# Kernel optimization log

Hardware: AMD Instinct MI355X
Metric: run time of the kernel (lower is better)

## Reference

```python
import jax, jax.numpy as jnp
import numpy as np

DIM = 320
DIM_HEAD = 10
HEADS = DIM // DIM_HEAD
WH, WW = 8, 8  # window_size
EPS = 1e-12    # F.normalize eps


def setup_inputs() -> dict:
    key = jax.random.key(0)
    ks = jax.random.split(key, 9)
    B, H, W, C = 8, 128, 128, DIM
    s = 0.02
    return {
        "x": jax.random.normal(ks[0], (B, H, W, C), jnp.float32),
        "qkv_w": jax.random.normal(ks[1], (C, 3 * C), jnp.float32) * s,
        "qkv_b": jax.random.normal(ks[2], (3 * C,), jnp.float32) * s,
        "proj_w": jax.random.normal(ks[3], (C, C), jnp.float32) * s,
        "proj_b": jax.random.normal(ks[4], (C,), jnp.float32) * s,
        "gamma": jnp.full((C,), 1e-5, jnp.float32),
        "w1": jax.random.normal(ks[5], (C, 4 * C), jnp.float32) * s,  # bias=False
        "w2": jax.random.normal(ks[6], (4 * C, C), jnp.float32) * s,
        "b2": jax.random.normal(ks[7], (C,), jnp.float32) * s,
    }


def _l2norm(v):
    # F.normalize(x, dim=-1): x / max(||x||_2, eps)
    n = jnp.sqrt(jnp.sum(v * v, axis=-1, keepdims=True))
    return v / jnp.maximum(n, EPS)


def _block(x, qkv_w, qkv_b, proj_w, proj_b, gamma, w1, w2, b2):
    x = _l2norm(x)
    B, H, W, C = x.shape
    # window partition: (B,H,W,C) -> (nW, WH, WW, C)
    xw = x.reshape(B, H // WH, WH, W // WW, WW, C)
    xw = xw.transpose(0, 1, 3, 2, 4, 5).reshape(-1, WH, WW, C)
    nW = xw.shape[0]
    N = WH * WW
    # attention (matches torch view: channels grouped as (heads, 3*dim_head))
    qkv = xw.reshape(nW, N, C) @ qkv_w + qkv_b           # (nW, N, 3C)
    qkv = qkv.reshape(nW, N, HEADS, 3 * DIM_HEAD).transpose(0, 2, 1, 3)
    q, k, v = jnp.split(qkv, 3, axis=-1)                 # each (nW, h, N, dh)
    scores = jnp.einsum("whnd,whmd->whnm", q, k) * (DIM_HEAD ** -0.5)
    attn = jax.nn.softmax(scores, axis=-1)
    o = jnp.einsum("whnm,whmd->whnd", attn, v)
    o = o.transpose(0, 2, 1, 3).reshape(nW, N, C) @ proj_w + proj_b
    xw = xw + o.reshape(nW, WH, WW, C)
    # window reverse
    x = xw.reshape(B, H // WH, W // WW, WH, WW, C)
    x = x.transpose(0, 1, 3, 2, 4, 5).reshape(B, H, W, C)
    x = _l2norm(x)
    h = jax.nn.relu(x @ w1)                              # (B,H,W,4C)
    h = jax.nn.relu(h @ w2 + b2)
    return x + h * gamma                                 # layerscale


def reference(x, qkv_w, qkv_b, proj_w, proj_b, gamma, w1, w2, b2):
    return _block(x, qkv_w, qkv_b, proj_w, proj_b, gamma, w1, w2, b2)
```

## Files before the change

kernel.cpp:

```cpp
#include <hip/hip_runtime.h>
#include <cstdint>

typedef __bf16 bf16;
typedef __attribute__((ext_vector_type(8))) __bf16 bf16x8;
typedef __attribute__((ext_vector_type(4))) float f32x4;
typedef __attribute__((ext_vector_type(4))) uint32_t u32x4;
typedef __attribute__((ext_vector_type(2))) uint32_t u32x2;

#define MTOT (8*128*128)
#define MCH  16384

#define GLOAD16(g, l) __builtin_amdgcn_global_load_lds( \
    (const __attribute__((address_space(1))) unsigned int*)(g), \
    (__attribute__((address_space(3))) unsigned int*)(l), 16, 0, 0)

__global__ __launch_bounds__(256)
void transpose_cast_kernel(const float* __restrict__ in, bf16* __restrict__ out,
                           int R, int C) {
    __shared__ float tile[32][33];
    const int tx = threadIdx.x & 31, ty = threadIdx.x >> 5;
    const int c0 = blockIdx.x * 32, r0 = blockIdx.y * 32;
#pragma unroll
    for (int r = ty; r < 32; r += 8) tile[r][tx] = in[(size_t)(r0 + r) * C + c0 + tx];
    __syncthreads();
#pragma unroll
    for (int r = ty; r < 32; r += 8) out[(size_t)(c0 + r) * R + r0 + tx] = (bf16)tile[tx][r];
}

__global__ __launch_bounds__(256)
void l2norm_kernel(const float* __restrict__ X, bf16* __restrict__ O) {
    const int tid = threadIdx.x, wv = tid >> 6, lane = tid & 63;
    const size_t row = (size_t)blockIdx.x * 4 + wv;
    const float* xr = X + row * 320;
    bf16* orow = O + row * 320;
    float v[5];
    float ss = 0.f;
#pragma unroll
    for (int r = 0; r < 5; ++r) {
        v[r] = xr[r * 64 + lane];
        ss += v[r] * v[r];
    }
#pragma unroll
    for (int off = 32; off; off >>= 1) ss += __shfl_xor(ss, off);
    const float sc = 1.f / fmaxf(sqrtf(ss), 1e-12f);
#pragma unroll
    for (int r = 0; r < 5; ++r) orow[r * 64 + lane] = (bf16)(v[r] * sc);
}

template <int WM, int WN, int EPI, typename OutT>
__global__ __launch_bounds__(WM * WN * 64)
void gemm_kernel(const bf16* __restrict__ A, const bf16* __restrict__ WT,
                 const float* __restrict__ bias, const bf16* __restrict__ res,
                 const float* __restrict__ gamma, OutT* __restrict__ out,
                 int K, int N) {
    constexpr int T  = WM * WN * 64;
    constexpr int BM = WM * 64, BN = WN * 64;
    constexpr int GA = (BM * 4) / T;
    constexpr int GB = (BN * 4) / T;
    constexpr int RG = T / 4;
    __shared__ bf16 As[BM * 32];
    __shared__ bf16 Bs[BN * 32];
    const int tid = threadIdx.x;
    const int wv = tid >> 6, lane = tid & 63;
    const int wm = wv / WN, wn = wv % WN;
    const int n0 = blockIdx.x * BN, m0 = blockIdx.y * BM;
    const int r0 = lane & 15, qd = lane >> 4;

    f32x4 acc[4][4];
#pragma unroll
    for (int i = 0; i < 4; ++i)
#pragma unroll
        for (int j = 0; j < 4; ++j)
#pragma unroll
            for (int r = 0; r < 4; ++r) acc[i][j][r] = 0.f;

    const int sr = tid >> 2, sc = (tid & 3) << 3;
    const bf16* Ag = A  + (size_t)(m0 + sr) * K + sc;
    const bf16* Bg = WT + (size_t)(n0 + sr) * K + sc;
    bf16* Asw = As + tid * 8;
    bf16* Bsw = Bs + tid * 8;
    const bf16* ap = As + (wm * 64 + r0) * 32 + qd * 8;
    const bf16* bp = Bs + (wn * 64 + r0) * 32 + qd * 8;

    for (int kk = 0; kk < K; kk += 32) {
        __syncthreads();
#pragma unroll
        for (int g = 0; g < GA; ++g)
            GLOAD16(Ag + (size_t)(g * RG) * K + kk, Asw + g * (T * 8));
#pragma unroll
        for (int g = 0; g < GB; ++g)
            GLOAD16(Bg + (size_t)(g * RG) * K + kk, Bsw + g * (T * 8));
        __syncthreads();
        bf16x8 a[4], b[4];
#pragma unroll
        for (int i = 0; i < 4; ++i) a[i] = *(const bf16x8*)(ap + i * (16 * 32));
#pragma unroll
        for (int j = 0; j < 4; ++j) b[j] = *(const bf16x8*)(bp + j * (16 * 32));
#pragma unroll
        for (int j = 0; j < 4; ++j)
#pragma unroll
            for (int i = 0; i < 4; ++i)
                acc[i][j] = __builtin_amdgcn_mfma_f32_16x16x32_bf16(a[i], b[j], acc[i][j], 0, 0, 0);
    }

#pragma unroll
    for (int i = 0; i < 4; ++i) {
        const int rb = m0 + wm * 64 + 16 * i + qd * 4;
#pragma unroll
        for (int j = 0; j < 4; ++j) {
            const int col = n0 + wn * 64 + 16 * j + r0;
            const float bv = (EPI != 1) ? bias[col] : 0.f;
            const float gv = (EPI == 2) ? gamma[col] : 0.f;
#pragma unroll
            for (int r = 0; r < 4; ++r) {
                const size_t row = (size_t)(rb + r);
                float v = acc[i][j][r];
                if (EPI == 0)      v += bv;
                else if (EPI == 1) v = fmaxf(v, 0.f);
                else               v = (float)res[row * (size_t)N + col] + fmaxf(v + bv, 0.f) * gv;
                out[row * (size_t)N + col] = (OutT)v;
            }
        }
    }
}

__global__ __launch_bounds__(256)
void attn_kernel(const bf16* __restrict__ QKV, bf16* __restrict__ AO) {
    __shared__ __align__(16) char smem[40960];
    const int tid = threadIdx.x, wv = tid >> 6, lane = tid & 63;
    const int p = blockIdx.x * 4 + wv;
    const int img = p >> 13, pi = p & 8191;
    const int w = pi >> 5, h = pi & 31;
    const int wh = w >> 4, ww = w & 15;
    const size_t tokbase = (size_t)img * 16384;
    const size_t tok = tokbase + (size_t)(wh * 8 + (lane >> 3)) * 128 + (ww * 8 + (lane & 7));

    char* reg = smem + wv * 10240;
    bf16* Vt  = (bf16*)reg;
    char* KaB = reg + 2048;
    char* QbB = reg + 6144;
    char* PaB = reg + 2048;
    float* invs = (float*)(reg + 1536);

    const uint32_t* qp = (const uint32_t*)(QKV + tok * 960 + h * 30);
    uint32_t rr[15];
#pragma unroll
    for (int d = 0; d < 15; ++d) rr[d] = qp[d];

    {
        const int swk = ((lane >> 1) & 3) << 4;
        u32x4 qc0 = {rr[0], rr[1], rr[2], rr[3]};
        u32x4 qc1 = {rr[4], 0u, 0u, 0u};
        u32x4 kc0 = {rr[5], rr[6], rr[7], rr[8]};
        u32x4 kc1 = {rr[9], 0u, 0u, 0u};
        u32x4 zc  = {0u, 0u, 0u, 0u};
        char* qr = QbB + lane * 64;
        char* kr = KaB + lane * 64;
        *(u32x4*)(qr + (0 ^ swk))  = qc0;
        *(u32x4*)(qr + (16 ^ swk)) = qc1;
        *(u32x4*)(qr + (32 ^ swk)) = zc;
        *(u32x4*)(qr + (48 ^ swk)) = zc;
        *(u32x4*)(kr + (0 ^ swk))  = kc0;
        *(u32x4*)(kr + (16 ^ swk)) = kc1;
        *(u32x4*)(kr + (32 ^ swk)) = zc;
        *(u32x4*)(kr + (48 ^ swk)) = zc;
#pragma unroll
        for (int e2 = 0; e2 < 5; ++e2) {
            const uint32_t dv = rr[10 + e2];
            const int e0 = 2 * e2, e1 = 2 * e2 + 1;
            *(uint16_t*)((char*)Vt + ((e0 * 128 + lane * 2) ^ ((e0 & 7) << 4))) = (uint16_t)(dv & 0xffffu);
            *(uint16_t*)((char*)Vt + ((e1 * 128 + lane * 2) ^ ((e1 & 7) << 4))) = (uint16_t)(dv >> 16);
        }
    }
    asm volatile("s_waitcnt lgkmcnt(0)" ::: "memory");
    __builtin_amdgcn_sched_barrier(0);

    const int r0 = lane & 15, qd = lane >> 4;

    f32x4 s[4][4];
#pragma unroll
    for (int i = 0; i < 4; ++i)
#pragma unroll
        for (int j = 0; j < 4; ++j)
#pragma unroll
            for (int r = 0; r < 4; ++r) s[i][j][r] = 0.f;
    {
        const int fro = (qd * 16) ^ (((r0 >> 1) & 3) << 4);
        bf16x8 ak[4], bq[4];
#pragma unroll
        for (int i = 0; i < 4; ++i) ak[i] = *(const bf16x8*)(KaB + (16 * i + r0) * 64 + fro);
#pragma unroll
        for (int j = 0; j < 4; ++j) bq[j] = *(const bf16x8*)(QbB + (16 * j + r0) * 64 + fro);
#pragma unroll
        for (int j = 0; j < 4; ++j)
#pragma unroll
            for (int i = 0; i < 4; ++i)
                s[i][j] = __builtin_amdgcn_mfma_f32_16x16x32_bf16(ak[i], bq[j], s[i][j], 0, 0, 0);
    }

    const float c = 0.31622776601683794f;
#pragma unroll
    for (int j = 0; j < 4; ++j) {
        float mx = s[0][j][0];
#pragma unroll
        for (int i = 0; i < 4; ++i)
#pragma unroll
            for (int r = 0; r < 4; ++r) mx = fmaxf(mx, s[i][j][r]);
        mx = fmaxf(mx, __shfl_xor(mx, 16));
        mx = fmaxf(mx, __shfl_xor(mx, 32));
        const float nb = -c * mx;
        float sum = 0.f;
#pragma unroll
        for (int i = 0; i < 4; ++i)
#pragma unroll
            for (int r = 0; r < 4; ++r) {
                const float pv = __expf(fmaf(s[i][j][r], c, nb));
                s[i][j][r] = pv;
                sum += pv;
            }
        sum += __shfl_xor(sum, 16);
        sum += __shfl_xor(sum, 32);
        if (qd == 0) invs[16 * j + r0] = 1.f / sum;
    }

#pragma unroll
    for (int j = 0; j < 4; ++j) {
        char* prow = PaB + (16 * j + r0) * 128;
        const int sw = (r0 & 7) << 4;
#pragma unroll
        for (int i = 0; i < 4; ++i) {
            const uint32_t b0 = __builtin_bit_cast(uint16_t, (bf16)s[i][j][0]);
            const uint32_t b1 = __builtin_bit_cast(uint16_t, (bf16)s[i][j][1]);
            const uint32_t b2 = __builtin_bit_cast(uint16_t, (bf16)s[i][j][2]);
            const uint32_t b3 = __builtin_bit_cast(uint16_t, (bf16)s[i][j][3]);
            u32x2 pk = {b0 | (b1 << 16), b2 | (b3 << 16)};
            *(u32x2*)(prow + ((32 * i + 8 * qd) ^ sw)) = pk;
        }
    }
    asm volatile("s_waitcnt lgkmcnt(0)" ::: "memory");
    __builtin_amdgcn_sched_barrier(0);

    f32x4 o[4];
#pragma unroll
    for (int i = 0; i < 4; ++i)
#pragma unroll
        for (int r = 0; r < 4; ++r) o[i][r] = 0.f;
    {
        const int swp = (r0 & 7) << 4;
#pragma unroll
        for (int kk = 0; kk < 2; ++kk) {
            const bf16x8 bV = *(const bf16x8*)((char*)Vt + ((r0 * 128 + kk * 64 + qd * 16) ^ swp));
#pragma unroll
            for (int i = 0; i < 4; ++i) {
                const bf16x8 aP = *(const bf16x8*)(PaB + (((16 * i + r0) * 128 + kk * 64 + qd * 16) ^ swp));
                o[i] = __builtin_amdgcn_mfma_f32_16x16x32_bf16(aP, bV, o[i], 0, 0, 0);
            }
        }
    }

#pragma unroll
    for (int i = 0; i < 4; ++i) {
        const f32x4 iv = *(const f32x4*)(invs + 16 * i + qd * 4);
#pragma unroll
        for (int r = 0; r < 4; ++r) {
            const int n = 16 * i + qd * 4 + r;
            const size_t tn = tokbase + (size_t)(wh * 8 + (n >> 3)) * 128 + (ww * 8 + (n & 7));
            if (r0 < 10)
                AO[tn * 320 + h * 10 + r0] = (bf16)(o[i][r] * iv[r]);
        }
    }
}

__global__ __launch_bounds__(256)
void proj_norm_kernel(const bf16* __restrict__ AO, const bf16* __restrict__ PT,
                      const float* __restrict__ pb, const bf16* XN, bf16* Z) {
    __shared__ bf16 As[64 * 32];
    __shared__ bf16 Bs[320 * 32];
    __shared__ float ssp[64][4];
    const int tid = threadIdx.x, wv = tid >> 6, lane = tid & 63;
    const int m0 = blockIdx.x * 64;
    const int r0 = lane & 15, qd = lane >> 4;

    f32x4 acc[4][5];
#pragma unroll
    for (int i = 0; i < 4; ++i)
#pragma unroll
        for (int j = 0; j < 5; ++j)
#pragma unroll
            for (int r = 0; r < 4; ++r) acc[i][j][r] = 0.f;

    const int sr = tid >> 2, sc = (tid & 3) << 3;
    const bf16* Ag = AO + (size_t)(m0 + sr) * 320 + sc;
    const bf16* Bg = PT + (size_t)sr * 320 + sc;

    for (int kk = 0; kk < 320; kk += 32) {
        __syncthreads();
        GLOAD16(Ag + kk, As + tid * 8);
#pragma unroll
        for (int g = 0; g < 5; ++g)
            GLOAD16(Bg + (size_t)(g * 64) * 320 + kk, Bs + g * 2048 + tid * 8);
        __syncthreads();
        bf16x8 a[4], b[5];
#pragma unroll
        for (int i = 0; i < 4; ++i) a[i] = *(const bf16x8*)(As + (16 * i + r0) * 32 + qd * 8);
#pragma unroll
        for (int j = 0; j < 5; ++j) b[j] = *(const bf16x8*)(Bs + (wv * 80 + 16 * j + r0) * 32 + qd * 8);
#pragma unroll
        for (int j = 0; j < 5; ++j)
#pragma unroll
            for (int i = 0; i < 4; ++i)
                acc[i][j] = __builtin_amdgcn_mfma_f32_16x16x32_bf16(a[i], b[j], acc[i][j], 0, 0, 0);
    }

#pragma unroll
    for (int i = 0; i < 4; ++i)
#pragma unroll
        for (int r = 0; r < 4; ++r) {
            const int row = 16 * i + qd * 4 + r;
            float ss = 0.f;
#pragma unroll
            for (int j = 0; j < 5; ++j) {
                const int col = wv * 80 + 16 * j + r0;
                float v = acc[i][j][r] + pb[col] + (float)XN[(size_t)(m0 + row) * 320 + col];
                acc[i][j][r] = v;
                ss += v * v;
            }
            ss += __shfl_xor(ss, 1);
            ss += __shfl_xor(ss, 2);
            ss += __shfl_xor(ss, 4);
            ss += __shfl_xor(ss, 8);
            if (r0 == 0) ssp[row][wv] = ss;
        }
    __syncthreads();
#pragma unroll
    for (int i = 0; i < 4; ++i)
#pragma unroll
        for (int r = 0; r < 4; ++r) {
            const int row = 16 * i + qd * 4 + r;
            const f32x4 sv = *(const f32x4*)ssp[row];
            const float sc2 = 1.f / fmaxf(sqrtf(sv[0] + sv[1] + sv[2] + sv[3]), 1e-12f);
#pragma unroll
            for (int j = 0; j < 5; ++j)
                Z[(size_t)(m0 + row) * 320 + wv * 80 + 16 * j + r0] = (bf16)(acc[i][j][r] * sc2);
        }
}

extern "C" void kernel_launch(void* const* d_in, const int* in_sizes, int n_in,
                              void* d_out, int out_size, void* d_ws, size_t ws_size,
                              hipStream_t stream) {
    (void)in_sizes; (void)n_in; (void)out_size;
    const float* x      = (const float*)d_in[0];
    const float* qkv_w  = (const float*)d_in[1];
    const float* qkv_b  = (const float*)d_in[2];
    const float* proj_w = (const float*)d_in[3];
    const float* proj_b = (const float*)d_in[4];
    const float* gamma  = (const float*)d_in[5];
    const float* w1     = (const float*)d_in[6];
    const float* w2     = (const float*)d_in[7];
    const float* b2     = (const float*)d_in[8];
    float* out = (float*)d_out;
    char* ws = (char*)d_ws;

    const size_t NEED_FULL = 83886080ull + 335544320ull + 83886080ull + 2457600ull;

    if (ws_size >= NEED_FULL) {
        bf16* XNb   = (bf16*)(ws);
        bf16* QKV_f = (bf16*)(ws + 83886080ull);
        bf16* H1_f  = QKV_f;
        bf16* AO_f  = (bf16*)(ws + 419430400ull);
        bf16* QT    = (bf16*)(ws + 503316480ull);
        bf16* PT    = QT + 960 * 320;
        bf16* W1T   = PT + 320 * 320;
        bf16* W2T   = W1T + 1280 * 320;

        transpose_cast_kernel<<<dim3(30, 10), 256, 0, stream>>>(qkv_w, QT, 320, 960);
        transpose_cast_kernel<<<dim3(10, 10), 256, 0, stream>>>(proj_w, PT, 320, 320);
        transpose_cast_kernel<<<dim3(40, 10), 256, 0, stream>>>(w1, W1T, 320, 1280);
        transpose_cast_kernel<<<dim3(10, 40), 256, 0, stream>>>(w2, W2T, 1280, 320);

        l2norm_kernel<<<MTOT / 4, 256, 0, stream>>>(x, XNb);

        gemm_kernel<4, 1, 0, bf16><<<dim3(15, MTOT / 256), 256, 0, stream>>>(
            XNb, QT, qkv_b, nullptr, nullptr, QKV_f, 320, 960);

        attn_kernel<<<(MTOT / 64 * 32) / 4, 256, 0, stream>>>(QKV_f, AO_f);

        proj_norm_kernel<<<MTOT / 64, 256, 0, stream>>>(AO_f, PT, proj_b, XNb, XNb);

        gemm_kernel<2, 2, 1, bf16><<<dim3(10, MTOT / 128), 256, 0, stream>>>(
            XNb, W1T, nullptr, nullptr, nullptr, H1_f, 320, 1280);

        gemm_kernel<2, 1, 2, float><<<dim3(5, MTOT / 128), 128, 0, stream>>>(
            H1_f, W2T, b2, XNb, gamma, out, 1280, 320);
    } else {
        bf16* XNb   = (bf16*)(ws);
        bf16* QKV_c = (bf16*)(ws + 10485760ull);
        bf16* H1_c  = QKV_c;
        bf16* AO_c  = (bf16*)(ws + 52428800ull);
        bf16* QT    = (bf16*)(ws + 62914560ull);
        bf16* PT    = QT + 960 * 320;
        bf16* W1T   = PT + 320 * 320;
        bf16* W2T   = W1T + 1280 * 320;

        transpose_cast_kernel<<<dim3(30, 10), 256, 0, stream>>>(qkv_w, QT, 320, 960);
        transpose_cast_kernel<<<dim3(10, 10), 256, 0, stream>>>(proj_w, PT, 320, 320);
        transpose_cast_kernel<<<dim3(40, 10), 256, 0, stream>>>(w1, W1T, 320, 1280);
        transpose_cast_kernel<<<dim3(10, 40), 256, 0, stream>>>(w2, W2T, 1280, 320);

        for (int c = 0; c < 8; ++c) {
            const float* x_c = x + (size_t)c * MCH * 320;
            float* out_c = out + (size_t)c * MCH * 320;

            l2norm_kernel<<<MCH / 4, 256, 0, stream>>>(x_c, XNb);

            gemm_kernel<4, 1, 0, bf16><<<dim3(15, MCH / 256), 256, 0, stream>>>(
                XNb, QT, qkv_b, nullptr, nullptr, QKV_c, 320, 960);

            attn_kernel<<<(256 * 32) / 4, 256, 0, stream>>>(QKV_c, AO_c);

            proj_norm_kernel<<<MCH / 64, 256, 0, stream>>>(AO_c, PT, proj_b, XNb, XNb);

            gemm_kernel<2, 2, 1, bf16><<<dim3(10, MCH / 128), 256, 0, stream>>>(
                XNb, W1T, nullptr, nullptr, nullptr, H1_c, 320, 1280);

            gemm_kernel<2, 1, 2, float><<<dim3(5, MCH / 128), 128, 0, stream>>>(
                H1_c, W2T, b2, XNb, gamma, out_c, 1280, 320);
        }
    }
}
```

Measured before the change: 1.185 ms.

## Replace GEMMs with double-buffered 64x320 wide-tile kernel shared by all stages

Unifies the QKV, projection+norm, MLP-up and MLP-down GEMMs into one templated kernel that computes a 64-row by 320-column output tile per block. It double-buffers the LDS staging so the next K-slice's global-to-LDS loads overlap the current MFMA work, with one barrier per iteration. The wider N tile changes A/B reuse and grid shapes, and the shared LDS footprint (two buffers of 320x32 B) grows, which may reduce occupancy.

```diff
diff --git a/kernel.cpp b/kernel.cpp
--- a/kernel.cpp
+++ b/kernel.cpp
@@ -47,78 +47,114 @@
     for (int r = 0; r < 5; ++r) orow[r * 64 + lane] = (bf16)(v[r] * sc);
 }
 
-template <int WM, int WN, int EPI, typename OutT>
-__global__ __launch_bounds__(WM * WN * 64)
-void gemm_kernel(const bf16* __restrict__ A, const bf16* __restrict__ WT,
-                 const float* __restrict__ bias, const bf16* __restrict__ res,
-                 const float* __restrict__ gamma, OutT* __restrict__ out,
-                 int K, int N) {
-    constexpr int T  = WM * WN * 64;
-    constexpr int BM = WM * 64, BN = WN * 64;
-    constexpr int GA = (BM * 4) / T;
-    constexpr int GB = (BN * 4) / T;
-    constexpr int RG = T / 4;
-    __shared__ bf16 As[BM * 32];
-    __shared__ bf16 Bs[BN * 32];
+template <int EPI, typename OutT>
+__global__ __launch_bounds__(256)
+void gemm_wide_kernel(const bf16* __restrict__ A, const bf16* __restrict__ WT,
+                      const float* __restrict__ bias, const bf16* __restrict__ res,
+                      const float* __restrict__ gamma, OutT* __restrict__ out,
+                      int K, int N) {
+    __shared__ bf16 As[2][64 * 32];
+    __shared__ bf16 Bs[2][320 * 32];
+    __shared__ float ssp[64][4];
     const int tid = threadIdx.x;
     const int wv = tid >> 6, lane = tid & 63;
-    const int wm = wv / WN, wn = wv % WN;
-    const int n0 = blockIdx.x * BN, m0 = blockIdx.y * BM;
+    const int n0 = blockIdx.x * 320;
+    const int m0 = blockIdx.y * 64;
     const int r0 = lane & 15, qd = lane >> 4;
 
-    f32x4 acc[4][4];
+    f32x4 acc[4][5];
 #pragma unroll
     for (int i = 0; i < 4; ++i)
 #pragma unroll
-        for (int j = 0; j < 4; ++j)
+        for (int j = 0; j < 5; ++j)
 #pragma unroll
             for (int r = 0; r < 4; ++r) acc[i][j][r] = 0.f;
 
     const int sr = tid >> 2, sc = (tid & 3) << 3;
     const bf16* Ag = A  + (size_t)(m0 + sr) * K + sc;
     const bf16* Bg = WT + (size_t)(n0 + sr) * K + sc;
-    bf16* Asw = As + tid * 8;
-    bf16* Bsw = Bs + tid * 8;
-    const bf16* ap = As + (wm * 64 + r0) * 32 + qd * 8;
-    const bf16* bp = Bs + (wn * 64 + r0) * 32 + qd * 8;
-
-    for (int kk = 0; kk < K; kk += 32) {
-        __syncthreads();
-#pragma unroll
-        for (int g = 0; g < GA; ++g)
-            GLOAD16(Ag + (size_t)(g * RG) * K + kk, Asw + g * (T * 8));
-#pragma unroll
-        for (int g = 0; g < GB; ++g)
-            GLOAD16(Bg + (size_t)(g * RG) * K + kk, Bsw + g * (T * 8));
-        __syncthreads();
-        bf16x8 a[4], b[4];
-#pragma unroll
-        for (int i = 0; i < 4; ++i) a[i] = *(const bf16x8*)(ap + i * (16 * 32));
-#pragma unroll
-        for (int j = 0; j < 4; ++j) b[j] = *(const bf16x8*)(bp + j * (16 * 32));
-#pragma unroll
-        for (int j = 0; j < 4; ++j)
+
+    auto STAGE = [&](int buf, int kkE) {
+        GLOAD16(Ag + kkE, &As[buf][tid * 8]);
+#pragma unroll
+        for (int g = 0; g < 5; ++g)
+            GLOAD16(Bg + (size_t)(g * 64) * K + kkE, &Bs[buf][g * 2048 + tid * 8]);
+    };
+
+    const int NT = K >> 5;
+    int cur = 0;
+    STAGE(0, 0);
+    __syncthreads();
+
+    for (int t = 0; t < NT; ++t) {
+        if (t + 1 < NT) STAGE(cur ^ 1, (t + 1) << 5);
+        bf16x8 a[4], b[5];
+#pragma unroll
+        for (int i = 0; i < 4; ++i)
+            a[i] = *(const bf16x8*)(&As[cur][(16 * i + r0) * 32 + qd * 8]);
+#pragma unroll
+        for (int j = 0; j < 5; ++j)
+            b[j] = *(const bf16x8*)(&Bs[cur][(wv * 80 + 16 * j + r0) * 32 + qd * 8]);
+#pragma unroll
+        for (int j = 0; j < 5; ++j)
 #pragma unroll
             for (int i = 0; i < 4; ++i)
                 acc[i][j] = __builtin_amdgcn_mfma_f32_16x16x32_bf16(a[i], b[j], acc[i][j], 0, 0, 0);
-    }
-
-#pragma unroll
-    for (int i = 0; i < 4; ++i) {
-        const int rb = m0 + wm * 64 + 16 * i + qd * 4;
-#pragma unroll
-        for (int j = 0; j < 4; ++j) {
-            const int col = n0 + wn * 64 + 16 * j + r0;
-            const float bv = (EPI != 1) ? bias[col] : 0.f;
-            const float gv = (EPI == 2) ? gamma[col] : 0.f;
+        __syncthreads();
+        cur ^= 1;
+    }
+
+    if (EPI == 3) {
+#pragma unroll
+        for (int i = 0; i < 4; ++i)
 #pragma unroll
             for (int r = 0; r < 4; ++r) {
-                const size_t row = (size_t)(rb + r);
-                float v = acc[i][j][r];
-                if (EPI == 0)      v += bv;
-                else if (EPI == 1) v = fmaxf(v, 0.f);
-                else               v = (float)res[row * (size_t)N + col] + fmaxf(v + bv, 0.f) * gv;
-                out[row * (size_t)N + col] = (OutT)v;
+                const int row = 16 * i + qd * 4 + r;
+                float ss2 = 0.f;
+#pragma unroll
+                for (int j = 0; j < 5; ++j) {
+                    const int col = wv * 80 + 16 * j + r0;
+                    float v = acc[i][j][r] + bias[col] + (float)res[(size_t)(m0 + row) * 320 + col];
+                    acc[i][j][r] = v;
+                    ss2 += v * v;
+                }
+                ss2 += __shfl_xor(ss2, 1);
+                ss2 += __shfl_xor(ss2, 2);
+                ss2 += __shfl_xor(ss2, 4);
+                ss2 += __shfl_xor(ss2, 8);
+                if (r0 == 0) ssp[row][wv] = ss2;
+            }
+        __syncthreads();
+#pragma unroll
+        for (int i = 0; i < 4; ++i)
+#pragma unroll
+            for (int r = 0; r < 4; ++r) {
+                const int row = 16 * i + qd * 4 + r;
+                const f32x4 sv = *(const f32x4*)ssp[row];
+                const float sc2 = 1.f / fmaxf(sqrtf(sv[0] + sv[1] + sv[2] + sv[3]), 1e-12f);
+#pragma unroll
+                for (int j = 0; j < 5; ++j)
+                    out[(size_t)(m0 + row) * 320 + wv * 80 + 16 * j + r0] =
+                        (OutT)(acc[i][j][r] * sc2);
+            }
+    } else {
+#pragma unroll
+        for (int i = 0; i < 4; ++i) {
+            const int rb = m0 + 16 * i + qd * 4;
+#pragma unroll
+            for (int j = 0; j < 5; ++j) {
+                const int col = n0 + wv * 80 + 16 * j + r0;
+                const float bv = (EPI != 1) ? bias[col] : 0.f;
+                const float gv = (EPI == 2) ? gamma[col] : 0.f;
+#pragma unroll
+                for (int r = 0; r < 4; ++r) {
+                    const size_t row = (size_t)(rb + r);
+                    float v = acc[i][j][r];
+                    if (EPI == 0)      v += bv;
+                    else if (EPI == 1) v = fmaxf(v, 0.f);
+                    else               v = (float)res[row * (size_t)N + col] + fmaxf(v + bv, 0.f) * gv;
+                    out[row * (size_t)N + col] = (OutT)v;
+                }
             }
         }
     }
@@ -271,80 +307,6 @@
     }
 }
 
-__global__ __launch_bounds__(256)
-void proj_norm_kernel(const bf16* __restrict__ AO, const bf16* __restrict__ PT,
-                      const float* __restrict__ pb, const bf16* XN, bf16* Z) {
-    __shared__ bf16 As[64 * 32];
-    __shared__ bf16 Bs[320 * 32];
-    __shared__ float ssp[64][4];
-    const int tid = threadIdx.x, wv = tid >> 6, lane = tid & 63;
-    const int m0 = blockIdx.x * 64;
-    const int r0 = lane & 15, qd = lane >> 4;
-
-    f32x4 acc[4][5];
-#pragma unroll
-    for (int i = 0; i < 4; ++i)
-#pragma unroll
-        for (int j = 0; j < 5; ++j)
-#pragma unroll
-            for (int r = 0; r < 4; ++r) acc[i][j][r] = 0.f;
-
-    const int sr = tid >> 2, sc = (tid & 3) << 3;
-    const bf16* Ag = AO + (size_t)(m0 + sr) * 320 + sc;
-    const bf16* Bg = PT + (size_t)sr * 320 + sc;
-
-    for (int kk = 0; kk < 320; kk += 32) {
-        __syncthreads();
-        GLOAD16(Ag + kk, As + tid * 8);
-#pragma unroll
-        for (int g = 0; g < 5; ++g)
-            GLOAD16(Bg + (size_t)(g * 64) * 320 + kk, Bs + g * 2048 + tid * 8);
-        __syncthreads();
-        bf16x8 a[4], b[5];
-#pragma unroll
-        for (int i = 0; i < 4; ++i) a[i] = *(const bf16x8*)(As + (16 * i + r0) * 32 + qd * 8);
-#pragma unroll
-        for (int j = 0; j < 5; ++j) b[j] = *(const bf16x8*)(Bs + (wv * 80 + 16 * j + r0) * 32 + qd * 8);
-#pragma unroll
-        for (int j = 0; j < 5; ++j)
-#pragma unroll
-            for (int i = 0; i < 4; ++i)
-                acc[i][j] = __builtin_amdgcn_mfma_f32_16x16x32_bf16(a[i], b[j], acc[i][j], 0, 0, 0);
-    }
-
-#pragma unroll
-    for (int i = 0; i < 4; ++i)
-#pragma unroll
-        for (int r = 0; r < 4; ++r) {
-            const int row = 16 * i + qd * 4 + r;
-            float ss = 0.f;
-#pragma unroll
-            for (int j = 0; j < 5; ++j) {
-                const int col = wv * 80 + 16 * j + r0;
-                float v = acc[i][j][r] + pb[col] + (float)XN[(size_t)(m0 + row) * 320 + col];
-                acc[i][j][r] = v;
-                ss += v * v;
-            }
-            ss += __shfl_xor(ss, 1);
-            ss += __shfl_xor(ss, 2);
-            ss += __shfl_xor(ss, 4);
-            ss += __shfl_xor(ss, 8);
-            if (r0 == 0) ssp[row][wv] = ss;
-        }
-    __syncthreads();
-#pragma unroll
-    for (int i = 0; i < 4; ++i)
-#pragma unroll
-        for (int r = 0; r < 4; ++r) {
-            const int row = 16 * i + qd * 4 + r;
-            const f32x4 sv = *(const f32x4*)ssp[row];
-            const float sc2 = 1.f / fmaxf(sqrtf(sv[0] + sv[1] + sv[2] + sv[3]), 1e-12f);
-#pragma unroll
-            for (int j = 0; j < 5; ++j)
-                Z[(size_t)(m0 + row) * 320 + wv * 80 + 16 * j + r0] = (bf16)(acc[i][j][r] * sc2);
-        }
-}
-
 extern "C" void kernel_launch(void* const* d_in, const int* in_sizes, int n_in,
                               void* d_out, int out_size, void* d_ws, size_t ws_size,
                               hipStream_t stream) {
@@ -380,17 +342,18 @@
 
         l2norm_kernel<<<MTOT / 4, 256, 0, stream>>>(x, XNb);
 
-        gemm_kernel<4, 1, 0, bf16><<<dim3(15, MTOT / 256), 256, 0, stream>>>(
+        gemm_wide_kernel<0, bf16><<<dim3(3, MTOT / 64), 256, 0, stream>>>(
             XNb, QT, qkv_b, nullptr, nullptr, QKV_f, 320, 960);
 
         attn_kernel<<<(MTOT / 64 * 32) / 4, 256, 0, stream>>>(QKV_f, AO_f);
 
-        proj_norm_kernel<<<MTOT / 64, 256, 0, stream>>>(AO_f, PT, proj_b, XNb, XNb);
-
-        gemm_kernel<2, 2, 1, bf16><<<dim3(10, MTOT / 128), 256, 0, stream>>>(
+        gemm_wide_kernel<3, bf16><<<dim3(1, MTOT / 64), 256, 0, stream>>>(
+            AO_f, PT, proj_b, XNb, nullptr, XNb, 320, 320);
+
+        gemm_wide_kernel<1, bf16><<<dim3(4, MTOT / 64), 256, 0, stream>>>(
             XNb, W1T, nullptr, nullptr, nullptr, H1_f, 320, 1280);
 
-        gemm_kernel<2, 1, 2, float><<<dim3(5, MTOT / 128), 128, 0, stream>>>(
+        gemm_wide_kernel<2, float><<<dim3(1, MTOT / 64), 256, 0, stream>>>(
             H1_f, W2T, b2, XNb, gamma, out, 1280, 320);
     } else {
         bf16* XNb   = (bf16*)(ws);
@@ -413,17 +376,18 @@
 
             l2norm_kernel<<<MCH / 4, 256, 0, stream>>>(x_c, XNb);
 
-            gemm_kernel<4, 1, 0, bf16><<<dim3(15, MCH / 256), 256, 0, stream>>>(
+            gemm_wide_kernel<0, bf16><<<dim3(3, MCH / 64), 256, 0, stream>>>(
                 XNb, QT, qkv_b, nullptr, nullptr, QKV_c, 320, 960);
 
             attn_kernel<<<(256 * 32) / 4, 256, 0, stream>>>(QKV_c, AO_c);
 
-            proj_norm_kernel<<<MCH / 64, 256, 0, stream>>>(AO_c, PT, proj_b, XNb, XNb);
-
-            gemm_kernel<2, 2, 1, bf16><<<dim3(10, MCH / 128), 256, 0, stream>>>(
+            gemm_wide_kernel<3, bf16><<<dim3(1, MCH / 64), 256, 0, stream>>>(
+                AO_c, PT, proj_b, XNb, nullptr, XNb, 320, 320);
+
+            gemm_wide_kernel<1, bf16><<<dim3(4, MCH / 64), 256, 0, stream>>>(
                 XNb, W1T, nullptr, nullptr, nullptr, H1_c, 320, 1280);
 
-            gemm_kernel<2, 1, 2, float><<<dim3(5, MCH / 128), 128, 0, stream>>>(
+            gemm_wide_kernel<2, float><<<dim3(1, MCH / 64), 256, 0, stream>>>(
                 H1_c, W2T, b2, XNb, gamma, out_c, 1280, 320);
         }
     }
```

Result: faster. 1.081 ms (-8.8%).
